# Optimization experiments

Hardware: AMD Instinct MI355X
Metric: run time of the kernel (lower is better)

The kernel has to match this reference:

```python
import jax, jax.numpy as jnp
import numpy as np

NEG_SLOPE = 0.2

def gat_conv(x, src, dst, n_nodes, W, a_src, a_dst, bias, heads, out_c):
    # x: [N, in]; W: [in, heads*out_c]; a_src/a_dst: [heads, out_c]; bias: [heads*out_c]
    h = (x @ W).reshape(n_nodes, heads, out_c)            # [N,H,C]
    e_s = jnp.sum(h * a_src, axis=-1)                     # [N,H] per-node src score
    e_d = jnp.sum(h * a_dst, axis=-1)                     # [N,H] per-node dst score
    e = jax.nn.leaky_relu(e_s[src] + e_d[dst], NEG_SLOPE) # [E,H]
    # segment softmax over destination neighborhoods
    emax = jax.ops.segment_max(e, dst, num_segments=n_nodes)  # [N,H]
    emax = jnp.where(jnp.isfinite(emax), emax, 0.0)
    p = jnp.exp(e - emax[dst])                            # [E,H]
    denom = jax.ops.segment_sum(p, dst, num_segments=n_nodes)  # [N,H]
    alpha = p / (denom[dst] + 1e-16)                      # [E,H]
    msg = h[src] * alpha[:, :, None]                      # [E,H,C]
    out = jax.ops.segment_sum(msg, dst, num_segments=n_nodes)  # [N,H,C]
    return out.reshape(n_nodes, heads * out_c) + bias


def setup_inputs() -> dict:
    key = jax.random.key(0)
    ks = jax.random.split(key, 10)
    N, E, IN, OUT, H = 50000, 1600000, 128, 32, 2
    x = jax.random.normal(ks[0], (N, IN), dtype=jnp.float32)
    edge_index = jax.random.randint(ks[1], (2, E), 0, N, dtype=jnp.int64)
    s = 0.1
    W1 = jax.random.normal(ks[2], (IN, H * OUT), dtype=jnp.float32) * s
    a_src1 = jax.random.normal(ks[3], (H, OUT), dtype=jnp.float32) * s
    a_dst1 = jax.random.normal(ks[4], (H, OUT), dtype=jnp.float32) * s
    b1 = jnp.zeros((H * OUT,), dtype=jnp.float32)
    W2 = jax.random.normal(ks[5], (H * OUT, OUT), dtype=jnp.float32) * s
    a_src2 = jax.random.normal(ks[6], (1, OUT), dtype=jnp.float32) * s
    a_dst2 = jax.random.normal(ks[7], (1, OUT), dtype=jnp.float32) * s
    b2 = jnp.zeros((OUT,), dtype=jnp.float32)
    return {"x": x, "edge_index": edge_index, "W1": W1, "a_src1": a_src1,
            "a_dst1": a_dst1, "b1": b1, "W2": W2, "a_src2": a_src2,
            "a_dst2": a_dst2, "b2": b2}


def reference(x, edge_index, W1, a_src1, a_dst1, b1, W2, a_src2, a_dst2, b2):
    N = x.shape[0]
    # add_self_loops=True (PyG GATConv default)
    loops = jnp.arange(N, dtype=edge_index.dtype)
    ei = jnp.concatenate([edge_index, jnp.stack([loops, loops])], axis=1)
    src, dst = ei[0], ei[1]
    h = gat_conv(x, src, dst, N, W1, a_src1, a_dst1, b1, heads=2, out_c=32)
    h = jax.nn.relu(h)
    out = gat_conv(h, src, dst, N, W2, a_src2, a_dst2, b2, heads=1, out_c=32)
    return out
```

## Files before the change

kernel.cpp:

```cpp
#include <hip/hip_runtime.h>
#include <hip/hip_fp16.h>

#define NEG_SLOPE 0.2f
#define DB 128
#define NB_MAX 512
#define EPB 4096
#define CAP 8192

__global__ __launch_bounds__(256) void k_g1p(
    const float* __restrict__ x, const float* __restrict__ W,
    const float* __restrict__ a_src, const float* __restrict__ a_dst,
    __half* __restrict__ h1, float* __restrict__ es, float* __restrict__ ed, int N,
    const int* __restrict__ srcv, const int* __restrict__ dstv,
    int* __restrict__ gcur, int* __restrict__ ebuf, int E, int G1) {
  __shared__ __align__(16) char smem[65536];
  const int t = threadIdx.x;

  if ((int)blockIdx.x < G1) {
    float* sXT = (float*)smem;
    float* sW  = (float*)(smem + 32768);
    const int r0 = blockIdx.x * 64;
    {
      const float4* Wp = (const float4*)W;
      float4* sWp = (float4*)sW;
#pragma unroll
      for (int i = 0; i < 8; ++i) sWp[t + i * 256] = Wp[t + i * 256];
    }
    {
      int r = t & 63;
      int kq = t >> 6;
      int gr = r0 + r;
      bool ok = gr < N;
      const float* xr = x + (size_t)gr * 128;
#pragma unroll
      for (int p = 0; p < 8; ++p) {
        int k = (kq + p * 4) * 4;
        float4 v = ok ? *(const float4*)(xr + k) : make_float4(0.f, 0.f, 0.f, 0.f);
        sXT[(k + 0) * 64 + r] = v.x;
        sXT[(k + 1) * 64 + r] = v.y;
        sXT[(k + 2) * 64 + r] = v.z;
        sXT[(k + 3) * 64 + r] = v.w;
      }
    }
    __syncthreads();

    const int tx = t & 15, ty = t >> 4;
    float4 acc0 = make_float4(0.f, 0.f, 0.f, 0.f);
    float4 acc1 = acc0, acc2 = acc0, acc3 = acc0;
#pragma unroll 8
    for (int k = 0; k < 128; ++k) {
      float4 av = *(const float4*)(sXT + k * 64 + ty * 4);
      float4 bv = *(const float4*)(sW + k * 64 + tx * 4);
      acc0.x += av.x * bv.x; acc0.y += av.x * bv.y; acc0.z += av.x * bv.z; acc0.w += av.x * bv.w;
      acc1.x += av.y * bv.x; acc1.y += av.y * bv.y; acc1.z += av.y * bv.z; acc1.w += av.y * bv.w;
      acc2.x += av.z * bv.x; acc2.y += av.z * bv.y; acc2.z += av.z * bv.z; acc2.w += av.z * bv.w;
      acc3.x += av.w * bv.x; acc3.y += av.w * bv.y; acc3.z += av.w * bv.z; acc3.w += av.w * bv.w;
    }

    float4 accs[4] = {acc0, acc1, acc2, acc3};
#pragma unroll
    for (int i = 0; i < 4; ++i) {
      int gr = r0 + ty * 4 + i;
      if (gr < N) {
        union { __half2 h[2]; float2 f; } u;
        u.h[0] = __float22half2_rn(make_float2(accs[i].x, accs[i].y));
        u.h[1] = __float22half2_rn(make_float2(accs[i].z, accs[i].w));
        *(float2*)(h1 + (size_t)gr * 64 + tx * 4) = u.f;
      }
    }

    float4 asv = *(const float4*)(a_src + tx * 4);
    float4 adv = *(const float4*)(a_dst + tx * 4);
    float esp[4], edp[4];
#pragma unroll
    for (int i = 0; i < 4; ++i) {
      esp[i] = accs[i].x * asv.x + accs[i].y * asv.y + accs[i].z * asv.z + accs[i].w * asv.w;
      edp[i] = accs[i].x * adv.x + accs[i].y * adv.y + accs[i].z * adv.z + accs[i].w * adv.w;
    }
#pragma unroll
    for (int off = 1; off <= 4; off <<= 1) {
#pragma unroll
      for (int i = 0; i < 4; ++i) {
        esp[i] += __shfl_xor(esp[i], off);
        edp[i] += __shfl_xor(edp[i], off);
      }
    }
    if ((tx & 7) == 0) {
      int hh = tx >> 3;
#pragma unroll
      for (int i = 0; i < 4; ++i) {
        int gr = r0 + ty * 4 + i;
        if (gr < N) {
          es[gr * 2 + hh] = esp[i];
          ed[gr * 2 + hh] = edp[i];
        }
      }
    }
  } else {
    int* sh    = (int*)smem;
    int* lbase = (int*)(smem + 2048);
    sh[t] = 0; sh[t + 256] = 0;
    __syncthreads();
    int base = (blockIdx.x - G1) * EPB;
    int dd[16];
#pragma unroll
    for (int i = 0; i < 16; ++i) {
      int e = base + i * 256 + t;
      dd[i] = (e < E) ? dstv[e] : -1;
      if (dd[i] >= 0) atomicAdd(&sh[dd[i] >> 7], 1);
    }
    __syncthreads();
#pragma unroll
    for (int i = 0; i < 2; ++i) {
      int b = t + 256 * i;
      int c = sh[b];
      lbase[b] = c ? (b * CAP + atomicAdd(&gcur[b], c)) : 0;
      sh[b] = 0;
    }
    __syncthreads();
#pragma unroll
    for (int i = 0; i < 16; ++i) {
      if (dd[i] >= 0) {
        int e = base + i * 256 + t;
        int b = dd[i] >> 7;
        int r = atomicAdd(&sh[b], 1);
        ebuf[lbase[b] + r] = srcv[e] | ((dd[i] & 127) << 16);
      }
    }
  }
}

__global__ __launch_bounds__(256) void k_csr(const int* __restrict__ gcur,
                                             const int* __restrict__ ebuf,
                                             int* __restrict__ rowbeg,
                                             int* __restrict__ rowend,
                                             unsigned short* __restrict__ col, int N) {
  int b = blockIdx.x;
  int cnt = gcur[b];
  int base = b * CAP;
  int dbase = b * DB;
  __shared__ int dh[DB];
  __shared__ int sc[DB];
  int t = threadIdx.x;
  if (t < DB) dh[t] = 0;
  __syncthreads();
  for (int j = t; j < cnt; j += 256) {
    int p = ebuf[base + j];
    atomicAdd(&dh[p >> 16], 1);
  }
  __syncthreads();
  int v = 0;
  if (t < DB) { v = dh[t]; sc[t] = v; }
  __syncthreads();
  for (int off = 1; off < DB; off <<= 1) {
    int u = 0;
    if (t < DB && t >= off) u = sc[t - off];
    __syncthreads();
    if (t < DB) sc[t] += u;
    __syncthreads();
  }
  if (t < DB) {
    int excl = sc[t] - v;
    int d = dbase + t;
    if (d < N) {
      rowbeg[d] = base + excl;
      rowend[d] = base + excl + v;
    }
    dh[t] = base + excl;
  }
  __syncthreads();
  for (int j = t; j < cnt; j += 256) {
    int p = ebuf[base + j];
    int r = atomicAdd(&dh[p >> 16], 1);
    col[r] = (unsigned short)(p & 0xFFFF);
  }
}

__global__ __launch_bounds__(256) void k_agg1(const int* __restrict__ rowbeg,
                                              const int* __restrict__ rowend,
                                              const unsigned short* __restrict__ col,
                                              const __half* __restrict__ h1,
                                              const float* __restrict__ es,
                                              const float* __restrict__ ed,
                                              const float* __restrict__ bias,
                                              float* __restrict__ out1, int N) {
  int d = (blockIdx.x * blockDim.x + threadIdx.x) >> 6;
  int lane = threadIdx.x & 63;
  if (d >= N) return;
  int g = lane >> 3;
  int q = lane & 7;
  int ch = q * 8;
  int hh = q >> 2;
  float edv = ed[d * 2 + hh];

  float a0 = 0.f, a1 = 0.f, a2 = 0.f, a3 = 0.f, a4 = 0.f, a5 = 0.f, a6 = 0.f, a7 = 0.f;
  float wsum = 0.f;

  if (g == 0) {
    float v = es[d * 2 + hh] + edv;
    v = v > 0.f ? v : NEG_SLOPE * v;
    float w = __expf(v);
    float4 raw = *(const float4*)(h1 + (size_t)d * 64 + ch);
    const __half2* p2 = (const __half2*)&raw;
    float2 f0 = __half22float2(p2[0]), f1 = __half22float2(p2[1]);
    float2 f2 = __half22float2(p2[2]), f3 = __half22float2(p2[3]);
    a0 = w * f0.x; a1 = w * f0.y; a2 = w * f1.x; a3 = w * f1.y;
    a4 = w * f2.x; a5 = w * f2.y; a6 = w * f3.x; a7 = w * f3.y;
    wsum = w;
  }

  int beg = rowbeg[d], end = rowend[d];
  for (int j = beg + g; j < end; j += 8) {
    int s = col[j];
    float vv = es[s * 2 + hh] + edv;
    vv = vv > 0.f ? vv : NEG_SLOPE * vv;
    float w = __expf(vv);
    float4 raw = *(const float4*)(h1 + (size_t)s * 64 + ch);
    const __half2* p2 = (const __half2*)&raw;
    float2 f0 = __half22float2(p2[0]), f1 = __half22float2(p2[1]);
    float2 f2 = __half22float2(p2[2]), f3 = __half22float2(p2[3]);
    a0 += w * f0.x; a1 += w * f0.y; a2 += w * f1.x; a3 += w * f1.y;
    a4 += w * f2.x; a5 += w * f2.y; a6 += w * f3.x; a7 += w * f3.y;
    wsum += w;
  }

#pragma unroll
  for (int off = 8; off <= 32; off <<= 1) {
    a0 += __shfl_xor(a0, off); a1 += __shfl_xor(a1, off);
    a2 += __shfl_xor(a2, off); a3 += __shfl_xor(a3, off);
    a4 += __shfl_xor(a4, off); a5 += __shfl_xor(a5, off);
    a6 += __shfl_xor(a6, off); a7 += __shfl_xor(a7, off);
    wsum += __shfl_xor(wsum, off);
  }

  if (g == 0) {
    float inv = 1.f / (wsum + 1e-16f);
    const float4 bv0 = *(const float4*)(bias + ch);
    const float4 bv1 = *(const float4*)(bias + ch + 4);
    float4 o0, o1;
    o0.x = a0 * inv + bv0.x; o0.y = a1 * inv + bv0.y;
    o0.z = a2 * inv + bv0.z; o0.w = a3 * inv + bv0.w;
    o1.x = a4 * inv + bv1.x; o1.y = a5 * inv + bv1.y;
    o1.z = a6 * inv + bv1.z; o1.w = a7 * inv + bv1.w;
    *(float4*)(out1 + (size_t)d * 64 + ch) = o0;
    *(float4*)(out1 + (size_t)d * 64 + ch + 4) = o1;
  }
}

__global__ __launch_bounds__(256) void k_gemm2(const float* __restrict__ out1,
                                               const float* __restrict__ W,
                                               const float* __restrict__ a_src,
                                               const float* __restrict__ a_dst,
                                               __half* __restrict__ hL2,
                                               float* __restrict__ es,
                                               float* __restrict__ ed, int N) {
  __shared__ float sXT[64 * 128];
  __shared__ float sW[64 * 32];
  const int t = threadIdx.x;
  const int r0 = blockIdx.x * 128;

  {
    const float4* Wp = (const float4*)W;
    float4* sWp = (float4*)sW;
#pragma unroll
    for (int i = 0; i < 2; ++i) sWp[t + i * 256] = Wp[t + i * 256];
  }
  {
    int r = t & 127;
    int kq = t >> 7;
    int gr = r0 + r;
    bool ok = gr < N;
    const float* xr = out1 + (size_t)gr * 64;
#pragma unroll
    for (int p = 0; p < 8; ++p) {
      int k = (kq + p * 2) * 4;
      float4 v = ok ? *(const float4*)(xr + k) : make_float4(0.f, 0.f, 0.f, 0.f);
      sXT[(k + 0) * 128 + r] = fmaxf(v.x, 0.f);
      sXT[(k + 1) * 128 + r] = fmaxf(v.y, 0.f);
      sXT[(k + 2) * 128 + r] = fmaxf(v.z, 0.f);
      sXT[(k + 3) * 128 + r] = fmaxf(v.w, 0.f);
    }
  }
  __syncthreads();

  const int tx = t & 7, ty = t >> 3;
  float4 acc0 = make_float4(0.f, 0.f, 0.f, 0.f);
  float4 acc1 = acc0, acc2 = acc0, acc3 = acc0;
#pragma unroll 8
  for (int k = 0; k < 64; ++k) {
    float4 av = *(const float4*)(sXT + k * 128 + ty * 4);
    float4 bv = *(const float4*)(sW + k * 32 + tx * 4);
    acc0.x += av.x * bv.x; acc0.y += av.x * bv.y; acc0.z += av.x * bv.z; acc0.w += av.x * bv.w;
    acc1.x += av.y * bv.x; acc1.y += av.y * bv.y; acc1.z += av.y * bv.z; acc1.w += av.y * bv.w;
    acc2.x += av.z * bv.x; acc2.y += av.z * bv.y; acc2.z += av.z * bv.z; acc2.w += av.z * bv.w;
    acc3.x += av.w * bv.x; acc3.y += av.w * bv.y; acc3.z += av.w * bv.z; acc3.w += av.w * bv.w;
  }

  float4 accs[4] = {acc0, acc1, acc2, acc3};
#pragma unroll
  for (int i = 0; i < 4; ++i) {
    int gr = r0 + ty * 4 + i;
    if (gr < N) {
      union { __half2 h[2]; float2 f; } u;
      u.h[0] = __float22half2_rn(make_float2(accs[i].x, accs[i].y));
      u.h[1] = __float22half2_rn(make_float2(accs[i].z, accs[i].w));
      *(float2*)(hL2 + (size_t)gr * 32 + tx * 4) = u.f;
    }
  }

  float4 asv = *(const float4*)(a_src + tx * 4);
  float4 adv = *(const float4*)(a_dst + tx * 4);
  float esp[4], edp[4];
#pragma unroll
  for (int i = 0; i < 4; ++i) {
    esp[i] = accs[i].x * asv.x + accs[i].y * asv.y + accs[i].z * asv.z + accs[i].w * asv.w;
    edp[i] = accs[i].x * adv.x + accs[i].y * adv.y + accs[i].z * adv.z + accs[i].w * adv.w;
  }
#pragma unroll
  for (int off = 1; off <= 4; off <<= 1) {
#pragma unroll
    for (int i = 0; i < 4; ++i) {
      esp[i] += __shfl_xor(esp[i], off);
      edp[i] += __shfl_xor(edp[i], off);
    }
  }
  if (tx == 0) {
#pragma unroll
    for (int i = 0; i < 4; ++i) {
      int gr = r0 + ty * 4 + i;
      if (gr < N) {
        es[gr] = esp[i];
        ed[gr] = edp[i];
      }
    }
  }
}

__global__ __launch_bounds__(256) void k_agg2(const int* __restrict__ rowbeg,
                                              const int* __restrict__ rowend,
                                              const unsigned short* __restrict__ col,
                                              const __half* __restrict__ hL2,
                                              const float* __restrict__ es,
                                              const float* __restrict__ ed,
                                              const float* __restrict__ bias,
                                              float* __restrict__ out, int N) {
  int d = (blockIdx.x * blockDim.x + threadIdx.x) >> 6;
  int lane = threadIdx.x & 63;
  if (d >= N) return;
  int g = lane >> 2;
  int q = lane & 3;
  int ch = q * 8;
  float edv = ed[d];

  float a0 = 0.f, a1 = 0.f, a2 = 0.f, a3 = 0.f, a4 = 0.f, a5 = 0.f, a6 = 0.f, a7 = 0.f;
  float wsum = 0.f;

  if (g == 0) {
    float v = es[d] + edv;
    v = v > 0.f ? v : NEG_SLOPE * v;
    float w = __expf(v);
    float4 raw = *(const float4*)(hL2 + (size_t)d * 32 + ch);
    const __half2* p2 = (const __half2*)&raw;
    float2 f0 = __half22float2(p2[0]), f1 = __half22float2(p2[1]);
    float2 f2 = __half22float2(p2[2]), f3 = __half22float2(p2[3]);
    a0 = w * f0.x; a1 = w * f0.y; a2 = w * f1.x; a3 = w * f1.y;
    a4 = w * f2.x; a5 = w * f2.y; a6 = w * f3.x; a7 = w * f3.y;
    wsum = w;
  }

  int beg = rowbeg[d], end = rowend[d];
  for (int j = beg + g; j < end; j += 16) {
    int s = col[j];
    float vv = es[s] + edv;
    vv = vv > 0.f ? vv : NEG_SLOPE * vv;
    float w = __expf(vv);
    float4 raw = *(const float4*)(hL2 + (size_t)s * 32 + ch);
    const __half2* p2 = (const __half2*)&raw;
    float2 f0 = __half22float2(p2[0]), f1 = __half22float2(p2[1]);
    float2 f2 = __half22float2(p2[2]), f3 = __half22float2(p2[3]);
    a0 += w * f0.x; a1 += w * f0.y; a2 += w * f1.x; a3 += w * f1.y;
    a4 += w * f2.x; a5 += w * f2.y; a6 += w * f3.x; a7 += w * f3.y;
    wsum += w;
  }

#pragma unroll
  for (int off = 4; off <= 32; off <<= 1) {
    a0 += __shfl_xor(a0, off); a1 += __shfl_xor(a1, off);
    a2 += __shfl_xor(a2, off); a3 += __shfl_xor(a3, off);
    a4 += __shfl_xor(a4, off); a5 += __shfl_xor(a5, off);
    a6 += __shfl_xor(a6, off); a7 += __shfl_xor(a7, off);
    wsum += __shfl_xor(wsum, off);
  }

  if (g == 0) {
    float inv = 1.f / (wsum + 1e-16f);
    const float4 bv0 = *(const float4*)(bias + ch);
    const float4 bv1 = *(const float4*)(bias + ch + 4);
    float4 o0, o1;
    o0.x = a0 * inv + bv0.x; o0.y = a1 * inv + bv0.y;
    o0.z = a2 * inv + bv0.z; o0.w = a3 * inv + bv0.w;
    o1.x = a4 * inv + bv1.x; o1.y = a5 * inv + bv1.y;
    o1.z = a6 * inv + bv1.z; o1.w = a7 * inv + bv1.w;
    *(float4*)(out + (size_t)d * 32 + ch) = o0;
    *(float4*)(out + (size_t)d * 32 + ch + 4) = o1;
  }
}

extern "C" void kernel_launch(void* const* d_in, const int* in_sizes, int n_in,
                              void* d_out, int out_size, void* d_ws, size_t ws_size,
                              hipStream_t stream) {
  const float* x      = (const float*)d_in[0];
  const int*   ei     = (const int*)d_in[1];
  const float* W1     = (const float*)d_in[2];
  const float* a_src1 = (const float*)d_in[3];
  const float* a_dst1 = (const float*)d_in[4];
  const float* b1     = (const float*)d_in[5];
  const float* W2     = (const float*)d_in[6];
  const float* a_src2 = (const float*)d_in[7];
  const float* a_dst2 = (const float*)d_in[8];
  const float* b2     = (const float*)d_in[9];
  float* out = (float*)d_out;

  const int N = in_sizes[0] / 128;
  const int E = in_sizes[1] / 2;
  const int NB = (N + DB - 1) / DB;
  const int* srcv = ei;
  const int* dstv = ei + E;

  char* base = (char*)d_ws;
  size_t off = 0;
  auto carve = [&](size_t bytes) {
    void* p = base + off;
    off += (bytes + 15) & ~(size_t)15;
    return p;
  };
  __half* h1     = (__half*)carve((size_t)N * 64 * 2);
  float*  es1    = (float*)carve((size_t)N * 2 * 4);
  float*  ed1    = (float*)carve((size_t)N * 2 * 4);
  float*  out1   = (float*)carve((size_t)N * 64 * 4);
  __half* hL2    = (__half*)carve((size_t)N * 32 * 2);
  float*  es2    = (float*)carve((size_t)N * 4);
  float*  ed2    = (float*)carve((size_t)N * 4);
  int*    gcur   = (int*)carve((size_t)NB_MAX * 4);
  int*    rowbeg = (int*)carve((size_t)N * 4);
  int*    rowend = (int*)carve((size_t)N * 4);
  unsigned short* col = (unsigned short*)carve((size_t)NB * CAP * 2);
  int*    ebuf   = (int*)carve((size_t)NB * CAP * 4);

  const int pblocks = (E + EPB - 1) / EPB;
  const int G1 = (N + 63) / 64;

  hipMemsetAsync(gcur, 0, (size_t)NB_MAX * sizeof(int), stream);

  k_g1p<<<G1 + pblocks, 256, 0, stream>>>(x, W1, a_src1, a_dst1, h1, es1, ed1, N,
                                          srcv, dstv, gcur, ebuf, E, G1);
  k_csr<<<NB, 256, 0, stream>>>(gcur, ebuf, rowbeg, rowend, col, N);

  k_agg1<<<((size_t)N * 64 + 255) / 256, 256, 0, stream>>>(rowbeg, rowend, col, h1, es1, ed1, b1, out1, N);

  k_gemm2<<<(N + 127) / 128, 256, 0, stream>>>(out1, W2, a_src2, a_dst2, hL2, es2, ed2, N);
  k_agg2<<<((size_t)N * 64 + 255) / 256, 256, 0, stream>>>(rowbeg, rowend, col, hL2, es2, ed2, b2, out, N);
}
```

Before: 213.9 us.

## Fuse layer-2 GEMM into layer-1 aggregation and store GEMM1 tiles as fp16

The layer-2 projection, ReLU and attention-score computation now run inside the layer-1 aggregation kernel, one wave per node, with W2 held in shared memory. This removes the separate GEMM2 launch and the fp32 out1 round trip through global memory. Separately, the first GEMM stages x and W1 in shared memory as fp16, halving its LDS footprint to allow more resident blocks, at the cost of reduced precision in h1. The fused aggregation adds a shared-memory matvec and extra shuffles per node, and relies on W2 being exactly 64x32.

```diff
diff --git a/kernel.cpp b/kernel.cpp
--- a/kernel.cpp
+++ b/kernel.cpp
@@ -13,18 +13,24 @@
     __half* __restrict__ h1, float* __restrict__ es, float* __restrict__ ed, int N,
     const int* __restrict__ srcv, const int* __restrict__ dstv,
     int* __restrict__ gcur, int* __restrict__ ebuf, int E, int G1) {
-  __shared__ __align__(16) char smem[65536];
+  __shared__ __align__(16) char smem[32768];
   const int t = threadIdx.x;
 
   if ((int)blockIdx.x < G1) {
-    float* sXT = (float*)smem;
-    float* sW  = (float*)(smem + 32768);
+    __half* sXT = (__half*)smem;
+    __half* sW  = (__half*)(smem + 16384);
     const int r0 = blockIdx.x * 64;
     {
       const float4* Wp = (const float4*)W;
-      float4* sWp = (float4*)sW;
-#pragma unroll
-      for (int i = 0; i < 8; ++i) sWp[t + i * 256] = Wp[t + i * 256];
+#pragma unroll
+      for (int i = 0; i < 8; ++i) {
+        float4 v = Wp[t + i * 256];
+        int fi = (t + i * 256) * 4;
+        union { __half2 h2[2]; float2 f; } u;
+        u.h2[0] = __float22half2_rn(make_float2(v.x, v.y));
+        u.h2[1] = __float22half2_rn(make_float2(v.z, v.w));
+        *(float2*)(sW + fi) = u.f;
+      }
     }
     {
       int r = t & 63;
@@ -36,10 +42,10 @@
       for (int p = 0; p < 8; ++p) {
         int k = (kq + p * 4) * 4;
         float4 v = ok ? *(const float4*)(xr + k) : make_float4(0.f, 0.f, 0.f, 0.f);
-        sXT[(k + 0) * 64 + r] = v.x;
-        sXT[(k + 1) * 64 + r] = v.y;
-        sXT[(k + 2) * 64 + r] = v.z;
-        sXT[(k + 3) * 64 + r] = v.w;
+        sXT[(k + 0) * 64 + r] = __float2half(v.x);
+        sXT[(k + 1) * 64 + r] = __float2half(v.y);
+        sXT[(k + 2) * 64 + r] = __float2half(v.z);
+        sXT[(k + 3) * 64 + r] = __float2half(v.w);
       }
     }
     __syncthreads();
@@ -47,14 +53,18 @@
     const int tx = t & 15, ty = t >> 4;
     float4 acc0 = make_float4(0.f, 0.f, 0.f, 0.f);
     float4 acc1 = acc0, acc2 = acc0, acc3 = acc0;
-#pragma unroll 8
+#pragma unroll 4
     for (int k = 0; k < 128; ++k) {
-      float4 av = *(const float4*)(sXT + k * 64 + ty * 4);
-      float4 bv = *(const float4*)(sW + k * 64 + tx * 4);
-      acc0.x += av.x * bv.x; acc0.y += av.x * bv.y; acc0.z += av.x * bv.z; acc0.w += av.x * bv.w;
-      acc1.x += av.y * bv.x; acc1.y += av.y * bv.y; acc1.z += av.y * bv.z; acc1.w += av.y * bv.w;
-      acc2.x += av.z * bv.x; acc2.y += av.z * bv.y; acc2.z += av.z * bv.z; acc2.w += av.z * bv.w;
-      acc3.x += av.w * bv.x; acc3.y += av.w * bv.y; acc3.z += av.w * bv.z; acc3.w += av.w * bv.w;
+      const __half2* ap = (const __half2*)(sXT + k * 64 + ty * 4);
+      const __half2* bp = (const __half2*)(sW + k * 64 + tx * 4);
+      float2 a01 = __half22float2(ap[0]);
+      float2 a23 = __half22float2(ap[1]);
+      float2 b01 = __half22float2(bp[0]);
+      float2 b23 = __half22float2(bp[1]);
+      acc0.x += a01.x * b01.x; acc0.y += a01.x * b01.y; acc0.z += a01.x * b23.x; acc0.w += a01.x * b23.y;
+      acc1.x += a01.y * b01.x; acc1.y += a01.y * b01.y; acc1.z += a01.y * b23.x; acc1.w += a01.y * b23.y;
+      acc2.x += a23.x * b01.x; acc2.y += a23.x * b01.y; acc2.z += a23.x * b23.x; acc2.w += a23.x * b23.y;
+      acc3.x += a23.y * b01.x; acc3.y += a23.y * b01.y; acc3.z += a23.y * b23.x; acc3.w += a23.y * b23.y;
     }
 
     float4 accs[4] = {acc0, acc1, acc2, acc3};
@@ -176,17 +186,32 @@
   }
 }
 
-__global__ __launch_bounds__(256) void k_agg1(const int* __restrict__ rowbeg,
-                                              const int* __restrict__ rowend,
-                                              const unsigned short* __restrict__ col,
-                                              const __half* __restrict__ h1,
-                                              const float* __restrict__ es,
-                                              const float* __restrict__ ed,
-                                              const float* __restrict__ bias,
-                                              float* __restrict__ out1, int N) {
-  int d = (blockIdx.x * blockDim.x + threadIdx.x) >> 6;
-  int lane = threadIdx.x & 63;
+__global__ __launch_bounds__(256) void k_agg1(
+    const int* __restrict__ rowbeg, const int* __restrict__ rowend,
+    const unsigned short* __restrict__ col,
+    const __half* __restrict__ h1,
+    const float* __restrict__ es, const float* __restrict__ ed,
+    const float* __restrict__ b1,
+    const float* __restrict__ W2,
+    const float* __restrict__ a_src2, const float* __restrict__ a_dst2,
+    __half* __restrict__ hL2, float* __restrict__ es2, float* __restrict__ ed2,
+    int N) {
+  __shared__ float sW2[64 * 32];
+  __shared__ float sRow[4 * 64];
+  const int t = threadIdx.x;
+  {
+    const float4* Wp = (const float4*)W2;
+    float4* sp = (float4*)sW2;
+    sp[t] = Wp[t];
+    sp[t + 256] = Wp[t + 256];
+  }
+  __syncthreads();
+
+  int d = (blockIdx.x * 256 + t) >> 6;
+  int lane = t & 63;
+  int wid = t >> 6;
   if (d >= N) return;
+
   int g = lane >> 3;
   int q = lane & 7;
   int ch = q * 8;
@@ -233,106 +258,39 @@
     wsum += __shfl_xor(wsum, off);
   }
 
+  float inv = 1.f / (wsum + 1e-16f);
   if (g == 0) {
-    float inv = 1.f / (wsum + 1e-16f);
-    const float4 bv0 = *(const float4*)(bias + ch);
-    const float4 bv1 = *(const float4*)(bias + ch + 4);
+    const float4 bv0 = *(const float4*)(b1 + ch);
+    const float4 bv1 = *(const float4*)(b1 + ch + 4);
     float4 o0, o1;
-    o0.x = a0 * inv + bv0.x; o0.y = a1 * inv + bv0.y;
-    o0.z = a2 * inv + bv0.z; o0.w = a3 * inv + bv0.w;
-    o1.x = a4 * inv + bv1.x; o1.y = a5 * inv + bv1.y;
-    o1.z = a6 * inv + bv1.z; o1.w = a7 * inv + bv1.w;
-    *(float4*)(out1 + (size_t)d * 64 + ch) = o0;
-    *(float4*)(out1 + (size_t)d * 64 + ch + 4) = o1;
-  }
-}
-
-__global__ __launch_bounds__(256) void k_gemm2(const float* __restrict__ out1,
-                                               const float* __restrict__ W,
-                                               const float* __restrict__ a_src,
-                                               const float* __restrict__ a_dst,
-                                               __half* __restrict__ hL2,
-                                               float* __restrict__ es,
-                                               float* __restrict__ ed, int N) {
-  __shared__ float sXT[64 * 128];
-  __shared__ float sW[64 * 32];
-  const int t = threadIdx.x;
-  const int r0 = blockIdx.x * 128;
-
-  {
-    const float4* Wp = (const float4*)W;
-    float4* sWp = (float4*)sW;
-#pragma unroll
-    for (int i = 0; i < 2; ++i) sWp[t + i * 256] = Wp[t + i * 256];
-  }
-  {
-    int r = t & 127;
-    int kq = t >> 7;
-    int gr = r0 + r;
-    bool ok = gr < N;
-    const float* xr = out1 + (size_t)gr * 64;
-#pragma unroll
-    for (int p = 0; p < 8; ++p) {
-      int k = (kq + p * 2) * 4;
-      float4 v = ok ? *(const float4*)(xr + k) : make_float4(0.f, 0.f, 0.f, 0.f);
-      sXT[(k + 0) * 128 + r] = fmaxf(v.x, 0.f);
-      sXT[(k + 1) * 128 + r] = fmaxf(v.y, 0.f);
-      sXT[(k + 2) * 128 + r] = fmaxf(v.z, 0.f);
-      sXT[(k + 3) * 128 + r] = fmaxf(v.w, 0.f);
-    }
-  }
-  __syncthreads();
-
-  const int tx = t & 7, ty = t >> 3;
-  float4 acc0 = make_float4(0.f, 0.f, 0.f, 0.f);
-  float4 acc1 = acc0, acc2 = acc0, acc3 = acc0;
-#pragma unroll 8
-  for (int k = 0; k < 64; ++k) {
-    float4 av = *(const float4*)(sXT + k * 128 + ty * 4);
-    float4 bv = *(const float4*)(sW + k * 32 + tx * 4);
-    acc0.x += av.x * bv.x; acc0.y += av.x * bv.y; acc0.z += av.x * bv.z; acc0.w += av.x * bv.w;
-    acc1.x += av.y * bv.x; acc1.y += av.y * bv.y; acc1.z += av.y * bv.z; acc1.w += av.y * bv.w;
-    acc2.x += av.z * bv.x; acc2.y += av.z * bv.y; acc2.z += av.z * bv.z; acc2.w += av.z * bv.w;
-    acc3.x += av.w * bv.x; acc3.y += av.w * bv.y; acc3.z += av.w * bv.z; acc3.w += av.w * bv.w;
-  }
-
-  float4 accs[4] = {acc0, acc1, acc2, acc3};
-#pragma unroll
-  for (int i = 0; i < 4; ++i) {
-    int gr = r0 + ty * 4 + i;
-    if (gr < N) {
-      union { __half2 h[2]; float2 f; } u;
-      u.h[0] = __float22half2_rn(make_float2(accs[i].x, accs[i].y));
-      u.h[1] = __float22half2_rn(make_float2(accs[i].z, accs[i].w));
-      *(float2*)(hL2 + (size_t)gr * 32 + tx * 4) = u.f;
-    }
-  }
-
-  float4 asv = *(const float4*)(a_src + tx * 4);
-  float4 adv = *(const float4*)(a_dst + tx * 4);
-  float esp[4], edp[4];
-#pragma unroll
-  for (int i = 0; i < 4; ++i) {
-    esp[i] = accs[i].x * asv.x + accs[i].y * asv.y + accs[i].z * asv.z + accs[i].w * asv.w;
-    edp[i] = accs[i].x * adv.x + accs[i].y * adv.y + accs[i].z * adv.z + accs[i].w * adv.w;
-  }
-#pragma unroll
-  for (int off = 1; off <= 4; off <<= 1) {
-#pragma unroll
-    for (int i = 0; i < 4; ++i) {
-      esp[i] += __shfl_xor(esp[i], off);
-      edp[i] += __shfl_xor(edp[i], off);
-    }
-  }
-  if (tx == 0) {
-#pragma unroll
-    for (int i = 0; i < 4; ++i) {
-      int gr = r0 + ty * 4 + i;
-      if (gr < N) {
-        es[gr] = esp[i];
-        ed[gr] = edp[i];
-      }
-    }
+    o0.x = fmaxf(a0 * inv + bv0.x, 0.f); o0.y = fmaxf(a1 * inv + bv0.y, 0.f);
+    o0.z = fmaxf(a2 * inv + bv0.z, 0.f); o0.w = fmaxf(a3 * inv + bv0.w, 0.f);
+    o1.x = fmaxf(a4 * inv + bv1.x, 0.f); o1.y = fmaxf(a5 * inv + bv1.y, 0.f);
+    o1.z = fmaxf(a6 * inv + bv1.z, 0.f); o1.w = fmaxf(a7 * inv + bv1.w, 0.f);
+    *(float4*)(sRow + wid * 64 + ch) = o0;
+    *(float4*)(sRow + wid * 64 + ch + 4) = o1;
+  }
+
+  int c = lane & 31, kh = lane >> 5;
+  const float* rp = sRow + wid * 64 + kh * 32;
+  const float* wp = sW2 + (kh * 32) * 32 + c;
+  float hv = 0.f;
+#pragma unroll
+  for (int k2 = 0; k2 < 32; ++k2) hv += rp[k2] * wp[k2 * 32];
+  hv += __shfl_xor(hv, 32);
+
+  float e_s = hv * a_src2[c];
+  float e_d = hv * a_dst2[c];
+#pragma unroll
+  for (int off = 1; off <= 16; off <<= 1) {
+    e_s += __shfl_xor(e_s, off);
+    e_d += __shfl_xor(e_d, off);
+  }
+  if (lane == 0) { es2[d] = e_s; ed2[d] = e_d; }
+
+  float hv2 = __shfl_xor(hv, 1);
+  if (lane < 32 && !(lane & 1)) {
+    *(__half2*)(hL2 + (size_t)d * 32 + c) = __float22half2_rn(make_float2(hv, hv2));
   }
 }
 
@@ -437,7 +395,6 @@
   __half* h1     = (__half*)carve((size_t)N * 64 * 2);
   float*  es1    = (float*)carve((size_t)N * 2 * 4);
   float*  ed1    = (float*)carve((size_t)N * 2 * 4);
-  float*  out1   = (float*)carve((size_t)N * 64 * 4);
   __half* hL2    = (__half*)carve((size_t)N * 32 * 2);
   float*  es2    = (float*)carve((size_t)N * 4);
   float*  ed2    = (float*)carve((size_t)N * 4);
@@ -456,8 +413,8 @@
                                           srcv, dstv, gcur, ebuf, E, G1);
   k_csr<<<NB, 256, 0, stream>>>(gcur, ebuf, rowbeg, rowend, col, N);
 
-  k_agg1<<<((size_t)N * 64 + 255) / 256, 256, 0, stream>>>(rowbeg, rowend, col, h1, es1, ed1, b1, out1, N);
-
-  k_gemm2<<<(N + 127) / 128, 256, 0, stream>>>(out1, W2, a_src2, a_dst2, hL2, es2, ed2, N);
+  k_agg1<<<((size_t)N * 64 + 255) / 256, 256, 0, stream>>>(
+      rowbeg, rowend, col, h1, es1, ed1, b1, W2, a_src2, a_dst2, hL2, es2, ed2, N);
+
   k_agg2<<<((size_t)N * 64 + 255) / 256, 256, 0, stream>>>(rowbeg, rowend, col, hL2, es2, ed2, b2, out, N);
 }
```

Measured after the change: 216.8 us. About the same (+1.3%).
